# Optimization experiments

Hardware: AMD Instinct MI355X
Metric: run time of the kernel (lower is better)

The kernel has to match this reference:

```python
import jax, jax.numpy as jnp
import numpy as np

N, S, C, K, V = 8, 8192, 1, 1024, 64  # batch, samples, n_channels, n_classes, vec_len


def setup_inputs() -> dict:
    key = jax.random.key(0)
    k1, k2 = jax.random.split(key)
    x0 = jax.random.normal(k1, (N, S, C, V), dtype=jnp.float32)
    embedding0 = jax.random.normal(k2, (C, K, V), dtype=jnp.float32) * 0.001
    return {"x0": x0, "embedding0": embedding0}


def reference(x0, embedding0):
    # normalize=False path of the original module
    x = x0
    emb = embedding0
    Ns = x.shape[0] * x.shape[1]
    xf = x.reshape(Ns, C, V)  # (Ns, C, V)
    # squared distances ||x - e||^2 without materializing (Ns, C, K, V)
    d2 = (
        jnp.sum(xf * xf, axis=-1)[:, :, None]
        - 2.0 * jnp.einsum("ncv,ckv->nck", xf, emb)
        + jnp.sum(emb * emb, axis=-1)[None, :, :]
    )
    index = jnp.argmin(d2, axis=2)  # (Ns, C); argmin of dist == argmin of dist^2
    # histogram entropy (matches torch histc over bins 0..K-1, divided by len(index)=Ns)
    counts = jnp.zeros((K,), jnp.float32).at[index.reshape(-1)].add(1.0)
    prob = counts / Ns
    safe_log = jnp.log(jnp.where(counts > 0, prob, 1.0))
    entropy = -jnp.sum(jnp.where(counts > 0, prob * safe_log, 0.0))
    # gather codewords: embedding[c, index[n,c]]
    output = emb[jnp.arange(C)[None, :], index].reshape(x.shape)
    out0 = jax.lax.stop_gradient(output - x) + x  # straight-through
    out1 = jnp.sum((jax.lax.stop_gradient(x) - output) ** 2, axis=-1)  # (N,S,C)
    out2 = jnp.sum((x - jax.lax.stop_gradient(output)) ** 2, axis=-1)  # (N,S,C)
    return (out0, out1, out2, entropy)
```

## Files before the change

kernel.cpp:

```cpp
#include <hip/hip_runtime.h>
#include <math.h>

#define NS   65536
#define KK   1024
#define VV   64
#define SPB  64
#define NB   (NS / SPB)
#define NW   8
#define TPW  2
#define NPASS 4
#define NMT  (SPB / 16)

#define OUT0_OFF 0
#define OUT1_OFF 4194304
#define OUT2_OFF 4259840
#define ENT_OFF  4325376


typedef __attribute__((ext_vector_type(8))) short bf16x8;
typedef __attribute__((ext_vector_type(4))) float f32x4;

__device__ __forceinline__ short f2bf(float f) {
    unsigned u = __float_as_uint(f);
    u = (u + 0x7fffu + ((u >> 16) & 1u)) >> 16;
    return (short)u;
}

__global__ void vq_prep(const float* __restrict__ emb, unsigned int* __restrict__ hist,
                        float* __restrict__ cinit, short* __restrict__ cb,
                        unsigned int* __restrict__ entCnt) {
    int t = blockIdx.x * blockDim.x + threadIdx.x;
    if (t == 0) entCnt[0] = 0u;
    if (t < KK) {
        hist[t] = 0u;
        const float4* e4 = (const float4*)(emb + (size_t)t * VV);
        const int T = t >> 4, cc = t & 15;
        float s = 0.f;
        union { short sh[8]; bf16x8 v; } pk;
        #pragma unroll
        for (int g = 0; g < 8; ++g) {
            float4 f0 = e4[2 * g], f1 = e4[2 * g + 1];
            s = fmaf(f0.x, f0.x, s); s = fmaf(f0.y, f0.y, s);
            s = fmaf(f0.z, f0.z, s); s = fmaf(f0.w, f0.w, s);
            s = fmaf(f1.x, f1.x, s); s = fmaf(f1.y, f1.y, s);
            s = fmaf(f1.z, f1.z, s); s = fmaf(f1.w, f1.w, s);
            pk.sh[0] = f2bf(f0.x); pk.sh[1] = f2bf(f0.y);
            pk.sh[2] = f2bf(f0.z); pk.sh[3] = f2bf(f0.w);
            pk.sh[4] = f2bf(f1.x); pk.sh[5] = f2bf(f1.y);
            pk.sh[6] = f2bf(f1.z); pk.sh[7] = f2bf(f1.w);
            short* dst = cb + (size_t)T * 1024 + (g >> 2) * 512 + ((g & 3) * 16 + cc) * 8;
            *(bf16x8*)dst = pk.v;
        }
        cinit[t] = 1.0f - 0.5f * s;
    }
}

__global__ __launch_bounds__(512, 4) void vq_main(
    const float* __restrict__ x, const float* __restrict__ emb,
    const float* __restrict__ cinit, const short* __restrict__ cb,
    unsigned int* __restrict__ hist,
    float* __restrict__ out0, float* __restrict__ out1, float* __restrict__ out2,
    float* __restrict__ entOut)
{
    __shared__ __align__(16) char  sA[SPB * 128];
    __shared__ float    sXn[SPB];
    __shared__ unsigned sRed[SPB][NW + 1];
    __shared__ unsigned sPkF[SPB];
    __shared__ float    sPart[NW];
    __shared__ unsigned sLast;

    const int tid  = threadIdx.x;
    const int lane = tid & 63;
    const int wv   = tid >> 6;
    const int col  = lane & 15;
    const int quad = lane >> 4;
    const int samp0 = blockIdx.x * SPB;

    {
        const int s = tid >> 3, g = tid & 7;
        const float* xp = x + (size_t)(samp0 + s) * VV + g * 8;
        float4 f0 = *(const float4*)(xp);
        float4 f1 = *(const float4*)(xp + 4);
        float sm = 0.f;
        sm=fmaf(f0.x,f0.x,sm); sm=fmaf(f0.y,f0.y,sm); sm=fmaf(f0.z,f0.z,sm); sm=fmaf(f0.w,f0.w,sm);
        sm=fmaf(f1.x,f1.x,sm); sm=fmaf(f1.y,f1.y,sm); sm=fmaf(f1.z,f1.z,sm); sm=fmaf(f1.w,f1.w,sm);
        union { short sh[8]; bf16x8 v; } pa;
        pa.sh[0]=f2bf(f0.x); pa.sh[1]=f2bf(f0.y); pa.sh[2]=f2bf(f0.z); pa.sh[3]=f2bf(f0.w);
        pa.sh[4]=f2bf(f1.x); pa.sh[5]=f2bf(f1.y); pa.sh[6]=f2bf(f1.z); pa.sh[7]=f2bf(f1.w);
        short* base = (short*)(sA + s * 128);
        *(bf16x8*)(base + ((g ^ (s & 7)) << 3)) = pa.v;
        sm += __shfl_xor(sm, 1, 64);
        sm += __shfl_xor(sm, 2, 64);
        sm += __shfl_xor(sm, 4, 64);
        if ((tid & 7) == 0) sXn[s] = sm;
    }

    const int rb0 = col * 128 + (( quad      ^ (col & 7)) << 4);
    const int rb1 = col * 128 + (((4 + quad) ^ (col & 7)) << 4);

    unsigned pmv[NMT];
    #pragma unroll
    for (int j = 0; j < NMT; ++j) pmv[j] = 0u;

    for (int p = 0; p < NPASS; ++p) {
        bf16x8   af0[TPW], af1[TPW];
        f32x4    cv[TPW];
        unsigned tg[TPW];
        const int Tb = p * 16 + wv * TPW;
        #pragma unroll
        for (int t = 0; t < TPW; ++t) {
            const char* cp = (const char*)cb + (size_t)(Tb + t) * 2048;
            af0[t] = *(const bf16x8*)(cp + lane * 16);
            af1[t] = *(const bf16x8*)(cp + 1024 + lane * 16);
            cv[t]  = *(const f32x4*)(cinit + (Tb + t) * 16 + quad * 4);
            tg[t]  = 1023u - (unsigned)((Tb + t) * 16 + quad * 4);
        }
        if (p == 0) __syncthreads();

        #pragma unroll
        for (int mt = 0; mt < NMT; ++mt) {
            const char* Bp = sA + mt * 2048;
            bf16x8 b0 = *(const bf16x8*)(Bp + rb0);
            bf16x8 b1 = *(const bf16x8*)(Bp + rb1);
            #pragma unroll
            for (int t = 0; t < TPW; ++t) {
                f32x4 acc = __builtin_amdgcn_mfma_f32_16x16x32_bf16(af0[t], b0, cv[t], 0, 0, 0);
                acc       = __builtin_amdgcn_mfma_f32_16x16x32_bf16(af1[t], b1, acc,   0, 0, 0);
                unsigned u0 = ((__float_as_uint(acc[0]) & 0xFFFFFC00u) | tg[t]);
                unsigned u1 = ((__float_as_uint(acc[1]) & 0xFFFFFC00u) | tg[t]) - 1u;
                unsigned u2 = ((__float_as_uint(acc[2]) & 0xFFFFFC00u) | tg[t]) - 2u;
                unsigned u3 = ((__float_as_uint(acc[3]) & 0xFFFFFC00u) | tg[t]) - 3u;
                unsigned m0 = u0 > u1 ? u0 : u1;
                unsigned m1 = u2 > u3 ? u2 : u3;
                unsigned mm = m0 > m1 ? m0 : m1;
                pmv[mt] = pmv[mt] > mm ? pmv[mt] : mm;
            }
        }
    }

    #pragma unroll
    for (int j = 0; j < NMT; ++j) {
        unsigned o;
        o = (unsigned)__shfl_xor((int)pmv[j], 16, 64); pmv[j] = o > pmv[j] ? o : pmv[j];
        o = (unsigned)__shfl_xor((int)pmv[j], 32, 64); pmv[j] = o > pmv[j] ? o : pmv[j];
    }
    {
        unsigned w0 = (quad & 1) ? pmv[1] : pmv[0];
        unsigned w1 = (quad & 1) ? pmv[3] : pmv[2];
        unsigned lo = (quad & 2) ? w1 : w0;
        sRed[quad * 16 + col][wv] = lo;
    }
    __syncthreads();

    if (tid < SPB) {
        unsigned pbest = sRed[tid][0];
        #pragma unroll
        for (int w = 1; w < NW; ++w) {
            unsigned o = sRed[tid][w];
            pbest = o > pbest ? o : pbest;
        }
        sPkF[tid] = pbest;
        int   code = 1023 - (int)(pbest & 1023u);
        float sf   = __uint_as_float(pbest & 0xFFFFFC00u);
        float d    = fmaf(-2.f, sf - 1.0f, sXn[tid]);
        int n = samp0 + tid;
        out1[n] = d;
        out2[n] = d;
        atomicAdd(&hist[code], 1u);
    }
    __syncthreads();

    {
        float4* dstB = (float4*)(out0 + (size_t)samp0 * VV);
        #pragma unroll
        for (int i = 0; i < 2; ++i) {
            const int idx  = i * 512 + tid;
            const int smp  = idx >> 4;
            const int part = idx & 15;
            const int code = 1023 - (int)(sPkF[smp] & 1023u);
            dstB[idx] = *((const float4*)(emb + (size_t)code * VV) + part);
        }
    }

    __syncthreads();
    unsigned int* entCnt = (unsigned int*)entOut;
    if (tid == 0) sLast = (atomicAdd(entCnt, 1u) == (NB - 1)) ? 1u : 0u;
    __syncthreads();
    if (sLast) {
        float e = 0.f;
        #pragma unroll
        for (int i = 0; i < 2; ++i) {
            unsigned c = atomicAdd(&hist[i * 512 + tid], 0u);
            if (c) { float pr = (float)c * (1.0f / (float)NS); e -= pr * logf(pr); }
        }
        #pragma unroll
        for (int off = 32; off > 0; off >>= 1) e += __shfl_down(e, off, 64);
        if (lane == 0) sPart[wv] = e;
        __syncthreads();
        if (tid == 0) {
            float s = 0.f;
            #pragma unroll
            for (int i = 0; i < NW; ++i) s += sPart[i];
            entOut[0] = s;
        }
    }
}

extern "C" void kernel_launch(void* const* d_in, const int* in_sizes, int n_in,
                              void* d_out, int out_size, void* d_ws, size_t ws_size,
                              hipStream_t stream) {
    const float* x   = (const float*)d_in[0];
    const float* emb = (const float*)d_in[1];
    float* out = (float*)d_out;
    unsigned int* hist  = (unsigned int*)d_ws;
    float*        cinit = (float*)((char*)d_ws + 4096);
    short*        cb    = (short*)((char*)d_ws + 8192);

    vq_prep<<<16, 64, 0, stream>>>(emb, hist, cinit, cb, (unsigned int*)(out + ENT_OFF));
    vq_main<<<NB, 512, 0, stream>>>(x, emb, cinit, cb, hist,
                                    out + OUT0_OFF, out + OUT1_OFF, out + OUT2_OFF,
                                    out + ENT_OFF);
}
```

Before: 93.39 us.

## Split entropy into separate kernel and widen codebook prep parallelism

The last-block atomic counter and in-kernel entropy reduction are replaced by a third small kernel that reads the histogram after the main kernel finishes. This removes two block-wide barriers and a global atomic from every main-kernel block. The prep kernel now uses eight threads per codeword with shuffle reductions instead of one thread per codeword, which spreads the codebook packing over more threads. In exchange it adds an extra kernel launch and its launch overhead.

```diff
diff --git a/kernel.cpp b/kernel.cpp
--- a/kernel.cpp
+++ b/kernel.cpp
@@ -27,47 +27,39 @@
 }
 
 __global__ void vq_prep(const float* __restrict__ emb, unsigned int* __restrict__ hist,
-                        float* __restrict__ cinit, short* __restrict__ cb,
-                        unsigned int* __restrict__ entCnt) {
-    int t = blockIdx.x * blockDim.x + threadIdx.x;
-    if (t == 0) entCnt[0] = 0u;
-    if (t < KK) {
-        hist[t] = 0u;
-        const float4* e4 = (const float4*)(emb + (size_t)t * VV);
-        const int T = t >> 4, cc = t & 15;
-        float s = 0.f;
-        union { short sh[8]; bf16x8 v; } pk;
-        #pragma unroll
-        for (int g = 0; g < 8; ++g) {
-            float4 f0 = e4[2 * g], f1 = e4[2 * g + 1];
-            s = fmaf(f0.x, f0.x, s); s = fmaf(f0.y, f0.y, s);
-            s = fmaf(f0.z, f0.z, s); s = fmaf(f0.w, f0.w, s);
-            s = fmaf(f1.x, f1.x, s); s = fmaf(f1.y, f1.y, s);
-            s = fmaf(f1.z, f1.z, s); s = fmaf(f1.w, f1.w, s);
-            pk.sh[0] = f2bf(f0.x); pk.sh[1] = f2bf(f0.y);
-            pk.sh[2] = f2bf(f0.z); pk.sh[3] = f2bf(f0.w);
-            pk.sh[4] = f2bf(f1.x); pk.sh[5] = f2bf(f1.y);
-            pk.sh[6] = f2bf(f1.z); pk.sh[7] = f2bf(f1.w);
-            short* dst = cb + (size_t)T * 1024 + (g >> 2) * 512 + ((g & 3) * 16 + cc) * 8;
-            *(bf16x8*)dst = pk.v;
-        }
-        cinit[t] = 1.0f - 0.5f * s;
-    }
+                        float* __restrict__ cinit, short* __restrict__ cb) {
+    const int t = blockIdx.x * blockDim.x + threadIdx.x;
+    const int c = t >> 3;
+    const int g = t & 7;
+    if (t < KK) hist[t] = 0u;
+    const float* ep = emb + (size_t)c * VV + g * 8;
+    float4 f0 = *(const float4*)(ep);
+    float4 f1 = *(const float4*)(ep + 4);
+    float s = 0.f;
+    s=fmaf(f0.x,f0.x,s); s=fmaf(f0.y,f0.y,s); s=fmaf(f0.z,f0.z,s); s=fmaf(f0.w,f0.w,s);
+    s=fmaf(f1.x,f1.x,s); s=fmaf(f1.y,f1.y,s); s=fmaf(f1.z,f1.z,s); s=fmaf(f1.w,f1.w,s);
+    union { short sh[8]; bf16x8 v; } pk;
+    pk.sh[0]=f2bf(f0.x); pk.sh[1]=f2bf(f0.y); pk.sh[2]=f2bf(f0.z); pk.sh[3]=f2bf(f0.w);
+    pk.sh[4]=f2bf(f1.x); pk.sh[5]=f2bf(f1.y); pk.sh[6]=f2bf(f1.z); pk.sh[7]=f2bf(f1.w);
+    const int T = c >> 4, cc = c & 15;
+    short* dst = cb + (size_t)T * 1024 + (g >> 2) * 512 + ((g & 3) * 16 + cc) * 8;
+    *(bf16x8*)dst = pk.v;
+    s += __shfl_xor(s, 1, 64);
+    s += __shfl_xor(s, 2, 64);
+    s += __shfl_xor(s, 4, 64);
+    if (g == 0) cinit[c] = 1.0f - 0.5f * s;
 }
 
 __global__ __launch_bounds__(512, 4) void vq_main(
     const float* __restrict__ x, const float* __restrict__ emb,
     const float* __restrict__ cinit, const short* __restrict__ cb,
     unsigned int* __restrict__ hist,
-    float* __restrict__ out0, float* __restrict__ out1, float* __restrict__ out2,
-    float* __restrict__ entOut)
+    float* __restrict__ out0, float* __restrict__ out1, float* __restrict__ out2)
 {
     __shared__ __align__(16) char  sA[SPB * 128];
     __shared__ float    sXn[SPB];
     __shared__ unsigned sRed[SPB][NW + 1];
     __shared__ unsigned sPkF[SPB];
-    __shared__ float    sPart[NW];
-    __shared__ unsigned sLast;
 
     const int tid  = threadIdx.x;
     const int lane = tid & 63;
@@ -181,28 +173,25 @@
             dstB[idx] = *((const float4*)(emb + (size_t)code * VV) + part);
         }
     }
-
+}
+
+__global__ void vq_ent(const unsigned int* __restrict__ hist, float* __restrict__ entOut) {
+    __shared__ float sPart[16];
+    const int tid  = threadIdx.x;
+    const int lane = tid & 63;
+    const int wv   = tid >> 6;
+    unsigned c = hist[tid];
+    float e = 0.f;
+    if (c) { float pr = (float)c * (1.0f / (float)NS); e = -pr * logf(pr); }
+    #pragma unroll
+    for (int off = 32; off > 0; off >>= 1) e += __shfl_down(e, off, 64);
+    if (lane == 0) sPart[wv] = e;
     __syncthreads();
-    unsigned int* entCnt = (unsigned int*)entOut;
-    if (tid == 0) sLast = (atomicAdd(entCnt, 1u) == (NB - 1)) ? 1u : 0u;
-    __syncthreads();
-    if (sLast) {
-        float e = 0.f;
-        #pragma unroll
-        for (int i = 0; i < 2; ++i) {
-            unsigned c = atomicAdd(&hist[i * 512 + tid], 0u);
-            if (c) { float pr = (float)c * (1.0f / (float)NS); e -= pr * logf(pr); }
-        }
-        #pragma unroll
-        for (int off = 32; off > 0; off >>= 1) e += __shfl_down(e, off, 64);
-        if (lane == 0) sPart[wv] = e;
-        __syncthreads();
-        if (tid == 0) {
-            float s = 0.f;
-            #pragma unroll
-            for (int i = 0; i < NW; ++i) s += sPart[i];
-            entOut[0] = s;
-        }
+    if (tid == 0) {
+        float s = 0.f;
+        #pragma unroll
+        for (int i = 0; i < 16; ++i) s += sPart[i];
+        entOut[0] = s;
     }
 }
 
@@ -216,8 +205,8 @@
     float*        cinit = (float*)((char*)d_ws + 4096);
     short*        cb    = (short*)((char*)d_ws + 8192);
 
-    vq_prep<<<16, 64, 0, stream>>>(emb, hist, cinit, cb, (unsigned int*)(out + ENT_OFF));
+    vq_prep<<<32, 256, 0, stream>>>(emb, hist, cinit, cb);
     vq_main<<<NB, 512, 0, stream>>>(x, emb, cinit, cb, hist,
-                                    out + OUT0_OFF, out + OUT1_OFF, out + OUT2_OFF,
-                                    out + ENT_OFF);
-}
+                                    out + OUT0_OFF, out + OUT1_OFF, out + OUT2_OFF);
+    vq_ent<<<1, 1024, 0, stream>>>(hist, out + ENT_OFF);
+}
```

After: 94.26 us. Within noise of the previous version (+0.9%).
